# Kernel optimization log

Measured on AMD Instinct MI355X. Metric: run time of the kernel, lower is better.

The kernel has to match this reference:

```python
import jax, jax.numpy as jnp
import numpy as np

B, N, C = 2, 2048, 768
H = 12
D = C // H
SCALE = D ** -0.5
EPS = 1e-5
HID = 4 * C


def layer_norm(x, g, b):
    mu = jnp.mean(x, axis=-1, keepdims=True)
    var = jnp.var(x, axis=-1, keepdims=True)
    return (x - mu) * jax.lax.rsqrt(var + EPS) * g + b


def setup_inputs():
    key = jax.random.key(0)
    ks = jax.random.split(key, 12)
    s = C ** -0.5
    x = jax.random.normal(ks[0], (B, N, C), dtype=jnp.float32)
    mask = (jax.random.uniform(ks[1], (B, N, N)) < 0.1).astype(jnp.float32)
    return {
        "x": x,
        "mask": mask,
        "g1": jnp.ones((C,), jnp.float32),
        "b1": jnp.zeros((C,), jnp.float32),
        "Wq": jax.random.normal(ks[2], (C, C), jnp.float32) * s,
        "Wkv": jax.random.normal(ks[3], (2 * C, C), jnp.float32) * s,
        "Wp": jax.random.normal(ks[4], (C, C), jnp.float32) * s,
        "bp": jnp.zeros((C,), jnp.float32),
        "g2": jnp.ones((C,), jnp.float32),
        "b2": jnp.zeros((C,), jnp.float32),
        "W1": jax.random.normal(ks[5], (HID, C), jnp.float32) * s,
        "bf1": jnp.zeros((HID,), jnp.float32),
        "W2": jax.random.normal(ks[6], (C, HID), jnp.float32) * (HID ** -0.5),
        "bf2": jnpmp if False else jnp.zeros((C,), jnp.float32),
    }


def block_fwd(x, mask, g1, b1, Wq, Wkv, Wp, bp, g2, b2, W1, bf1, W2, bf2):
    # --- attention branch (pre-norm) ---
    xn = layer_norm(x, g1, b1)
    q = (xn @ Wq.T).reshape(B, N, H, D).transpose(0, 2, 1, 3)      # bhnd
    kv = (xn @ Wkv.T).reshape(B, N, 2, H, D).transpose(2, 0, 3, 1, 4)
    k, v = kv[0], kv[1]                                             # bhnd
    attn = jnp.einsum('bhnd,bhmd->bhnm', q, k) * SCALE
    attn = attn + (mask * -100000.0)[:, None]                       # additive mask
    attn = jax.nn.softmax(attn, axis=-1)
    o = jnp.einsum('bhnm,bhmd->bhnd', attn, v)
    o = o.transpose(0, 2, 1, 3).reshape(B, N, C)
    o = o @ Wp.T + bp
    x = x + o
    # --- MLP branch (pre-norm) ---
    xn2 = layer_norm(x, g2, b2)
    h = jax.nn.gelu(xn2 @ W1.T + bf1, approximate=False)
    x = x + (h @ W2.T + bf2)
    return x


def reference(x, mask, g1, b1, Wq, Wkv, Wp, bp, g2, b2, W1, bf1, W2, bf2):
    return block_fwd(x, mask, g1, b1, Wq, Wkv, Wp, bp, g2, b2, W1, bf1, W2, bf2)
```

## Files before the change

kernel.cpp:

```cpp
#include <hip/hip_runtime.h>
#include <hip/hip_bf16.h>
#include <cstdint>
#include <cstddef>

#define BB 2
#define NN 2048
#define CC 768
#define HH 12
#define DD 64
#define HID 3072
#define TT (BB*NN)

typedef __attribute__((ext_vector_type(8))) short bf16x8;
typedef __attribute__((ext_vector_type(4))) short bf16x4;
typedef __attribute__((ext_vector_type(4))) float f32x4;

__device__ __forceinline__ unsigned short f2bf(float f) {
    unsigned int u = __float_as_uint(f);
    u += 0x7fffu + ((u >> 16) & 1u);
    return (unsigned short)(u >> 16);
}
__device__ __forceinline__ float bf2f(unsigned short u) {
    return __uint_as_float(((unsigned int)u) << 16);
}
#if __has_builtin(__builtin_amdgcn_exp2f)
#define EXP2F(x) __builtin_amdgcn_exp2f(x)
#else
#define EXP2F(x) exp2f(x)
#endif

__device__ __forceinline__ void gload16(const void* g, void* l) {
    __builtin_amdgcn_global_load_lds((__attribute__((address_space(1))) unsigned int*)g,
                                     (__attribute__((address_space(3))) unsigned int*)l,
                                     16, 0, 0);
}

__device__ __forceinline__ void barrier_lgkm() {
    asm volatile("s_waitcnt lgkmcnt(0)" ::: "memory");
    __builtin_amdgcn_s_barrier();
}

struct CvtArgs {
    const float* in[5];
    unsigned short* out[5];
    int n4[5];
};
typedef __attribute__((ext_vector_type(4))) float float4v;
typedef __attribute__((ext_vector_type(4))) unsigned short ushort4v;
__global__ __launch_bounds__(256) void cvt5_kernel(CvtArgs a) {
    int base = blockIdx.x * 256 + threadIdx.x;
    int stride = gridDim.x * 256;
#pragma unroll
    for (int s = 0; s < 5; ++s) {
        const float4v* ip = (const float4v*)a.in[s];
        ushort4v* op = (ushort4v*)a.out[s];
        for (int i = base; i < a.n4[s]; i += stride) {
            float4v v = ip[i];
            ushort4v o;
            o[0] = f2bf(v[0]); o[1] = f2bf(v[1]); o[2] = f2bf(v[2]); o[3] = f2bf(v[3]);
            op[i] = o;
        }
    }
}

__global__ __launch_bounds__(256) void maskbits_kernel(const float* __restrict__ mask,
                                                       unsigned short* __restrict__ mb, int n) {
    int i = blockIdx.x * 256 + threadIdx.x;
    if (i >= n) return;
    const float4v* mp = (const float4v*)(mask + (size_t)i * 16);
    unsigned int bits = 0;
#pragma unroll
    for (int q = 0; q < 4; ++q) {
        float4v v = mp[q];
#pragma unroll
        for (int j = 0; j < 4; ++j) bits |= (v[j] > 0.5f) ? (1u << (q * 4 + j)) : 0u;
    }
    mb[i] = (unsigned short)bits;
}

__global__ __launch_bounds__(256) void ln_kernel(const float* __restrict__ x,
                                                 const float* __restrict__ g,
                                                 const float* __restrict__ b,
                                                 unsigned short* __restrict__ out) {
    int t = blockIdx.x;
    int tid = threadIdx.x;
    const float* xr = x + (size_t)t * CC;
    float v0 = xr[tid], v1 = xr[tid + 256], v2 = xr[tid + 512];
    float s = v0 + v1 + v2;
    float s2 = v0 * v0 + v1 * v1 + v2 * v2;
#pragma unroll
    for (int off = 1; off < 64; off <<= 1) {
        s  += __shfl_xor(s, off);
        s2 += __shfl_xor(s2, off);
    }
    __shared__ float red[8];
    int wv = tid >> 6, lane = tid & 63;
    if (lane == 0) { red[wv] = s; red[wv + 4] = s2; }
    __syncthreads();
    s  = red[0] + red[1] + red[2] + red[3];
    s2 = red[4] + red[5] + red[6] + red[7];
    float mu   = s * (1.0f / CC);
    float var  = s2 * (1.0f / CC) - mu * mu;
    float rstd = rsqrtf(var + 1e-5f);
    unsigned short* orow = out + (size_t)t * CC;
    orow[tid]       = f2bf((v0 - mu) * rstd * g[tid]       + b[tid]);
    orow[tid + 256] = f2bf((v1 - mu) * rstd * g[tid + 256] + b[tid + 256]);
    orow[tid + 512] = f2bf((v2 - mu) * rstd * g[tid + 512] + b[tid + 512]);
}

template <int EPI, int BM>
__global__ __launch_bounds__(256) void gemm_bt(const unsigned short* __restrict__ A,
                                               const unsigned short* __restrict__ Bw,
                                               const float* __restrict__ bias,
                                               const float* __restrict__ res,
                                               void* __restrict__ out,
                                               int M, int N, int K) {
    constexpr int MI = BM / 32;
    __shared__ alignas(16) unsigned short As[BM * 32];
    __shared__ alignas(16) unsigned short Bs[128 * 32];
    int tid = threadIdx.x;
    int lane = tid & 63, wv = tid >> 6;
    int l16 = lane & 15, lg = lane >> 4;
    int bm = blockIdx.x, bn = blockIdx.y;
    int wm = (wv & 1) * (BM / 2), wn = (wv >> 1) * 64;

    f32x4 acc[MI][4];
#pragma unroll
    for (int i = 0; i < MI; ++i)
#pragma unroll
        for (int j = 0; j < 4; ++j) acc[i][j] = f32x4{0.f, 0.f, 0.f, 0.f};

    const unsigned short* Ab = A + (size_t)bm * BM * K;
    const unsigned short* Bb = Bw + (size_t)bn * 128 * K;

    for (int k0 = 0; k0 < K; k0 += 32) {
        __syncthreads();
        constexpr int NCA = (BM * 4) / 256;
#pragma unroll
        for (int i = 0; i < NCA; ++i) {
            int c = tid + i * 256;
            int row = c >> 2, cc = (c & 3) * 8;
            gload16(Ab + (size_t)row * K + k0 + cc, &As[c * 8]);
        }
#pragma unroll
        for (int i = 0; i < 2; ++i) {
            int c = tid + i * 256;
            int row = c >> 2, cc = (c & 3) * 8;
            gload16(Bb + (size_t)row * K + k0 + cc, &Bs[c * 8]);
        }
        __syncthreads();
        bf16x8 af[MI], bfr[4];
#pragma unroll
        for (int mi = 0; mi < MI; ++mi) af[mi]  = *(const bf16x8*)&As[(wm + mi * 16 + l16) * 32 + lg * 8];
#pragma unroll
        for (int ni = 0; ni < 4; ++ni) bfr[ni] = *(const bf16x8*)&Bs[(wn + ni * 16 + l16) * 32 + lg * 8];
#pragma unroll
        for (int mi = 0; mi < MI; ++mi)
#pragma unroll
            for (int ni = 0; ni < 4; ++ni)
                acc[mi][ni] = __builtin_amdgcn_mfma_f32_16x16x32_bf16(af[mi], bfr[ni], acc[mi][ni], 0, 0, 0);
    }

#pragma unroll
    for (int ni = 0; ni < 4; ++ni) {
        int col = bn * 128 + wn + ni * 16 + l16;
        float bv = (EPI == 0) ? 0.f : bias[col];
#pragma unroll
        for (int mi = 0; mi < MI; ++mi) {
#pragma unroll
            for (int r = 0; r < 4; ++r) {
                int row = bm * BM + wm + mi * 16 + lg * 4 + r;
                float v = acc[mi][ni][r];
                size_t idx = (size_t)row * N + col;
                if (EPI == 0) {
                    ((unsigned short*)out)[idx] = f2bf(v);
                } else if (EPI == 1) {
                    ((float*)out)[idx] = v + bv + res[idx];
                } else if (EPI == 2) {
                    v += bv;
                    v = 0.5f * v * (1.0f + erff(v * 0.70710678118f));
                    ((unsigned short*)out)[idx] = f2bf(v);
                } else {
                    ((float*)out)[idx] = v + bv + res[idx];
                }
            }
        }
    }
}

#define KVB 64
#define ANT (NN/KVB)
#define VP 68
__global__ __launch_bounds__(256) void attn_kernel(const unsigned short* __restrict__ qkv,
                                                   const unsigned short* __restrict__ maskb,
                                                   unsigned short* __restrict__ o) {
    __shared__ alignas(16) unsigned short Ks[2][64 * 64];
    __shared__ alignas(16) unsigned short Vt[2][64 * VP];
    int tid = threadIdx.x;
    int lane = tid & 63, wv = tid >> 6;
    int l16 = lane & 15, lg = lane >> 4;
    int qb = blockIdx.x;
    int bh = blockIdx.y;
    int b = bh / HH, h = bh % HH;
    int qrow = qb * 64 + wv * 16 + l16;

    const unsigned short* qp = qkv + ((size_t)(b * NN + qrow)) * 2304 + h * DD;
    bf16x8 q0r = *(const bf16x8*)(qp + 8 * lg);
    bf16x8 q1r = *(const bf16x8*)(qp + 32 + 8 * lg);
    const float QSC = 0.125f * 1.4426950408889634f;
    bf16x8 q0, q1;
#pragma unroll
    for (int j = 0; j < 8; ++j) {
        q0[j] = (short)f2bf(bf2f((unsigned short)q0r[j]) * QSC);
        q1[j] = (short)f2bf(bf2f((unsigned short)q1r[j]) * QSC);
    }

    const unsigned short* mrow  = maskb + ((size_t)(b * NN + qrow)) * 128;
    const unsigned short* kbase = qkv + (size_t)b * NN * 2304 + 768 + h * DD;
    const unsigned short* vbase = qkv + (size_t)b * NN * 2304 + 1536 + h * DD;

    int kc1_row = tid >> 3, kc7 = tid & 7;
    int kc2_row = kc1_row + 32;
    int klds1 = kc1_row * 64 + ((kc7 ^ (kc1_row & 7)) * 8);
    int klds2 = kc2_row * 64 + ((kc7 ^ (kc2_row & 7)) * 8);
    int kp = tid & 31, dg = tid >> 5;

    int sw = l16 & 7;
    int kb0 = l16 * 64 + ((lg ^ sw) * 8);
    int kb1 = l16 * 64 + (((lg + 4) ^ sw) * 8);
    int vbo = l16 * VP + lg * 4;

    bf16x8 ka, kb, va, vb;
    unsigned long long mb_cur, mb_nxt;

    f32x4 oa[4];
#pragma unroll
    for (int i = 0; i < 4; ++i) oa[i] = f32x4{0.f, 0.f, 0.f, 0.f};
    float mrun = -INFINITY, lrun = 0.f;

    auto LOAD = [&](int t) {
        ka = *(const bf16x8*)(kbase + (size_t)(t * KVB + kc1_row) * 2304 + kc7 * 8);
        kb = *(const bf16x8*)(kbase + (size_t)(t * KVB + kc2_row) * 2304 + kc7 * 8);
        va = *(const bf16x8*)(vbase + (size_t)(t * KVB + 2 * kp) * 2304 + dg * 8);
        vb = *(const bf16x8*)(vbase + (size_t)(t * KVB + 2 * kp + 1) * 2304 + dg * 8);
        mb_nxt = *(const unsigned long long*)(mrow + t * 4);
    };
    auto WRITE = [&](int s) {
        unsigned short* Kd = Ks[s];
        *(bf16x8*)&Kd[klds1] = ka;
        *(bf16x8*)&Kd[klds2] = kb;
        unsigned int* VtU = (unsigned int*)Vt[s];
#pragma unroll
        for (int j = 0; j < 8; ++j)
            VtU[(dg * 8 + j) * (VP / 2) + kp] =
                (unsigned int)(unsigned short)va[j] | ((unsigned int)(unsigned short)vb[j] << 16);
    };

    LOAD(0);
    WRITE(0);
    mb_cur = mb_nxt;
    int cur = 0;

    for (int kt = 0; kt < ANT; ++kt) {
        bool pre = (kt + 1 < ANT);
        if (pre) LOAD(kt + 1);
        barrier_lgkm();
        const unsigned short* Ksc = Ks[cur];
        const unsigned short* Vtc = Vt[cur];

        float sv[16];
#pragma unroll
        for (int ks = 0; ks < 4; ++ks) {
            bf16x8 k0 = *(const bf16x8*)&Ksc[kb0 + ks * 1024];
            bf16x8 k1 = *(const bf16x8*)&Ksc[kb1 + ks * 1024];
            f32x4 sa = f32x4{0.f, 0.f, 0.f, 0.f};
            sa = __builtin_amdgcn_mfma_f32_16x16x32_bf16(k0, q0, sa, 0, 0, 0);
            sa = __builtin_amdgcn_mfma_f32_16x16x32_bf16(k1, q1, sa, 0, 0, 0);
            unsigned int m16 = (unsigned int)(mb_cur >> (ks * 16 + lg * 4));
#pragma unroll
            for (int r = 0; r < 4; ++r) {
                float mbit = (float)((m16 >> r) & 1u);
                sv[ks * 4 + r] = fmaf(mbit, -144269.5f, sa[r]);
            }
        }
        float tmax = sv[0];
#pragma unroll
        for (int i = 1; i < 16; ++i) tmax = fmaxf(tmax, sv[i]);
        tmax = fmaxf(tmax, __shfl_xor(tmax, 16));
        tmax = fmaxf(tmax, __shfl_xor(tmax, 32));

        if (__any(tmax > mrun + 11.5f)) {
            float mnew = fmaxf(mrun, tmax);
            float sc = EXP2F(mrun - mnew);
            lrun *= sc;
#pragma unroll
            for (int db = 0; db < 4; ++db) {
                oa[db][0] *= sc; oa[db][1] *= sc; oa[db][2] *= sc; oa[db][3] *= sc;
            }
            mrun = mnew;
        }

        float ps = 0.f;
        bf16x4 pf[4];
#pragma unroll
        for (int ks = 0; ks < 4; ++ks)
#pragma unroll
            for (int r = 0; r < 4; ++r) {
                float p = EXP2F(sv[ks * 4 + r] - mrun);
                ps += p;
                pf[ks][r] = (short)f2bf(p);
            }
        lrun += ps;

#pragma unroll
        for (int ks = 0; ks < 4; ++ks)
#pragma unroll
            for (int db = 0; db < 4; ++db) {
                bf16x4 vf = *(const bf16x4*)&Vtc[vbo + db * 16 * VP + ks * 16];
                oa[db] = __builtin_amdgcn_mfma_f32_16x16x16bf16_1k(vf, pf[ks], oa[db], 0, 0, 0);
            }

        barrier_lgkm();
        if (pre) { WRITE(cur ^ 1); cur ^= 1; mb_cur = mb_nxt; }
    }

    float lt = lrun;
    lt += __shfl_xor(lt, 16);
    lt += __shfl_xor(lt, 32);
    float inv = 1.0f / lt;
    unsigned short* op = o + ((size_t)(b * NN + qrow)) * CC + h * DD;
#pragma unroll
    for (int db = 0; db < 4; ++db) {
        bf16x4 ov;
#pragma unroll
        for (int r = 0; r < 4; ++r) ov[r] = (short)f2bf(oa[db][r] * inv);
        *(bf16x4*)&op[db * 16 + lg * 4] = ov;
    }
}

extern "C" void kernel_launch(void* const* d_in, const int* in_sizes, int n_in,
                              void* d_out, int out_size, void* d_ws, size_t ws_size,
                              hipStream_t stream) {
    const float* x    = (const float*)d_in[0];
    const float* mask = (const float*)d_in[1];
    const float* g1   = (const float*)d_in[2];
    const float* b1   = (const float*)d_in[3];
    const float* Wq   = (const float*)d_in[4];
    const float* Wkv  = (const float*)d_in[5];
    const float* Wp   = (const float*)d_in[6];
    const float* bp   = (const float*)d_in[7];
    const float* g2   = (const float*)d_in[8];
    const float* b2   = (const float*)d_in[9];
    const float* W1   = (const float*)d_in[10];
    const float* bf1  = (const float*)d_in[11];
    const float* W2   = (const float*)d_in[12];
    const float* bf2  = (const float*)d_in[13];
    float* out = (float*)d_out;

    char* w = (char*)d_ws;
    unsigned short* wqkv = (unsigned short*)w;      w += (size_t)2304 * 768 * 2;
    unsigned short* wp   = (unsigned short*)w;      w += (size_t)768 * 768 * 2;
    unsigned short* w1   = (unsigned short*)w;      w += (size_t)3072 * 768 * 2;
    unsigned short* w2   = (unsigned short*)w;      w += (size_t)768 * 3072 * 2;
    unsigned short* xn   = (unsigned short*)w;      w += (size_t)TT * CC * 2;
    unsigned short* qkv  = (unsigned short*)w;      w += (size_t)TT * 2304 * 2;
    unsigned short* mb   = (unsigned short*)w;      w += (size_t)BB * NN * 128 * 2;
    unsigned short* obuf = (unsigned short*)w;      w += (size_t)TT * CC * 2;
    float*          x1   = (float*)w;               w += (size_t)TT * CC * 4;
    unsigned short* xn2  = (unsigned short*)w;      w += (size_t)TT * CC * 2;
    unsigned short* hbuf = (unsigned short*)w;      w += (size_t)TT * HID * 2;

    CvtArgs ca;
    ca.in[0] = Wq;  ca.out[0] = wqkv;             ca.n4[0] = 768 * 768 / 4;
    ca.in[1] = Wkv; ca.out[1] = wqkv + 768 * 768; ca.n4[1] = 1536 * 768 / 4;
    ca.in[2] = Wp;  ca.out[2] = wp;               ca.n4[2] = 768 * 768 / 4;
    ca.in[3] = W1;  ca.out[3] = w1;               ca.n4[3] = 3072 * 768 / 4;
    ca.in[4] = W2;  ca.out[4] = w2;               ca.n4[4] = 768 * 3072 / 4;
    cvt5_kernel<<<1024, 256, 0, stream>>>(ca);

    {
        int n = BB * NN * (NN / 16);
        maskbits_kernel<<<(n + 255) / 256, 256, 0, stream>>>(mask, mb, n);
    }

    ln_kernel<<<TT, 256, 0, stream>>>(x, g1, b1, xn);

    gemm_bt<0, 128><<<dim3(TT / 128, 2304 / 128), 256, 0, stream>>>(xn, wqkv, nullptr, nullptr, qkv, TT, 2304, 768);

    attn_kernel<<<dim3(NN / 64, BB * HH), 256, 0, stream>>>(qkv, mb, obuf);

    gemm_bt<1, 64><<<dim3(TT / 64, 768 / 128), 256, 0, stream>>>(obuf, wp, bp, x, x1, TT, 768, 768);

    ln_kernel<<<TT, 256, 0, stream>>>(x1, g2, b2, xn2);

    gemm_bt<2, 128><<<dim3(TT / 128, HID / 128), 256, 0, stream>>>(xn2, w1, bf1, nullptr, hbuf, TT, HID, 768);

    gemm_bt<3, 64><<<dim3(TT / 64, 768 / 128), 256, 0, stream>>>(hbuf, w2, bf2, x1, out, TT, 768, HID);
}
```

Before: 226.8 us.

## Double-buffer GEMM LDS with swizzle and widen attention to 512 threads

The GEMM now double-buffers its A/B LDS tiles, issuing the next k-slice's direct-to-LDS loads before computing the current one, and XOR-swizzles the column chunks to cut LDS bank conflicts. It needs one barrier per iteration instead of two. The attention kernel moves to 512-thread blocks covering 128 query rows, which halves K/V tile loads per query. K tiles now go straight to LDS via global_load_lds, while V is still transposed through registers. This costs more LDS per GEMM block and larger attention blocks, which can lower occupancy, and it depends on the global_load_lds completing before the __syncthreads.

```diff
diff --git a/kernel.cpp b/kernel.cpp
--- a/kernel.cpp
+++ b/kernel.cpp
@@ -33,11 +33,6 @@
     __builtin_amdgcn_global_load_lds((__attribute__((address_space(1))) unsigned int*)g,
                                      (__attribute__((address_space(3))) unsigned int*)l,
                                      16, 0, 0);
-}
-
-__device__ __forceinline__ void barrier_lgkm() {
-    asm volatile("s_waitcnt lgkmcnt(0)" ::: "memory");
-    __builtin_amdgcn_s_barrier();
 }
 
 struct CvtArgs {
@@ -116,49 +111,69 @@
                                                void* __restrict__ out,
                                                int M, int N, int K) {
     constexpr int MI = BM / 32;
-    __shared__ alignas(16) unsigned short As[BM * 32];
-    __shared__ alignas(16) unsigned short Bs[128 * 32];
+    constexpr int NCA = (BM * 4) / 256;
+    __shared__ alignas(16) unsigned short As[2][BM * 32];
+    __shared__ alignas(16) unsigned short Bs[2][128 * 32];
     int tid = threadIdx.x;
     int lane = tid & 63, wv = tid >> 6;
     int l16 = lane & 15, lg = lane >> 4;
     int bm = blockIdx.x, bn = blockIdx.y;
     int wm = (wv & 1) * (BM / 2), wn = (wv >> 1) * 64;
 
-    f32x4 acc[MI][4];
-#pragma unroll
-    for (int i = 0; i < MI; ++i)
-#pragma unroll
-        for (int j = 0; j < 4; ++j) acc[i][j] = f32x4{0.f, 0.f, 0.f, 0.f};
-
     const unsigned short* Ab = A + (size_t)bm * BM * K;
     const unsigned short* Bb = Bw + (size_t)bn * 128 * K;
 
-    for (int k0 = 0; k0 < K; k0 += 32) {
-        __syncthreads();
-        constexpr int NCA = (BM * 4) / 256;
-#pragma unroll
-        for (int i = 0; i < NCA; ++i) {
-            int c = tid + i * 256;
-            int row = c >> 2, cc = (c & 3) * 8;
-            gload16(Ab + (size_t)row * K + k0 + cc, &As[c * 8]);
-        }
-#pragma unroll
-        for (int i = 0; i < 2; ++i) {
-            int c = tid + i * 256;
-            int row = c >> 2, cc = (c & 3) * 8;
-            gload16(Bb + (size_t)row * K + k0 + cc, &Bs[c * 8]);
-        }
-        __syncthreads();
+    const unsigned short* aSrc[NCA]; int aDst[NCA];
+#pragma unroll
+    for (int i = 0; i < NCA; ++i) {
+        int c = tid + i * 256;
+        int row = c >> 2, p = c & 3;
+        int lc = p ^ ((row >> 1) & 3);
+        aSrc[i] = Ab + (size_t)row * K + lc * 8;
+        aDst[i] = c * 8;
+    }
+    const unsigned short* bSrc[2]; int bDst[2];
+#pragma unroll
+    for (int i = 0; i < 2; ++i) {
+        int c = tid + i * 256;
+        int row = c >> 2, p = c & 3;
+        int lc = p ^ ((row >> 1) & 3);
+        bSrc[i] = Bb + (size_t)row * K + lc * 8;
+        bDst[i] = c * 8;
+    }
+    int aoff = (wm + l16) * 32 + ((lg ^ (((wm + l16) >> 1) & 3)) * 8);
+    int boff = (wn + l16) * 32 + ((lg ^ (((wn + l16) >> 1) & 3)) * 8);
+
+    f32x4 acc[MI][4];
+#pragma unroll
+    for (int i = 0; i < MI; ++i)
+#pragma unroll
+        for (int j = 0; j < 4; ++j) acc[i][j] = f32x4{0.f, 0.f, 0.f, 0.f};
+
+    auto STAGE = [&](int s, int k0) {
+#pragma unroll
+        for (int i = 0; i < NCA; ++i) gload16(aSrc[i] + k0, &As[s][aDst[i]]);
+#pragma unroll
+        for (int i = 0; i < 2; ++i)   gload16(bSrc[i] + k0, &Bs[s][bDst[i]]);
+    };
+
+    STAGE(0, 0);
+    __syncthreads();
+    int nt = K / 32;
+    for (int t = 0; t < nt; ++t) {
+        int cur = t & 1;
+        if (t + 1 < nt) STAGE(cur ^ 1, (t + 1) * 32);
         bf16x8 af[MI], bfr[4];
 #pragma unroll
-        for (int mi = 0; mi < MI; ++mi) af[mi]  = *(const bf16x8*)&As[(wm + mi * 16 + l16) * 32 + lg * 8];
-#pragma unroll
-        for (int ni = 0; ni < 4; ++ni) bfr[ni] = *(const bf16x8*)&Bs[(wn + ni * 16 + l16) * 32 + lg * 8];
+        for (int mi = 0; mi < MI; ++mi) af[mi]  = *(const bf16x8*)&As[cur][aoff + mi * 512];
+#pragma unroll
+        for (int ni = 0; ni < 4; ++ni)  bfr[ni] = *(const bf16x8*)&Bs[cur][boff + ni * 512];
 #pragma unroll
         for (int mi = 0; mi < MI; ++mi)
 #pragma unroll
             for (int ni = 0; ni < 4; ++ni)
                 acc[mi][ni] = __builtin_amdgcn_mfma_f32_16x16x32_bf16(af[mi], bfr[ni], acc[mi][ni], 0, 0, 0);
+        __syncthreads();
     }
 
 #pragma unroll
@@ -191,7 +206,7 @@
 #define KVB 64
 #define ANT (NN/KVB)
 #define VP 68
-__global__ __launch_bounds__(256) void attn_kernel(const unsigned short* __restrict__ qkv,
+__global__ __launch_bounds__(512) void attn_kernel(const unsigned short* __restrict__ qkv,
                                                    const unsigned short* __restrict__ maskb,
                                                    unsigned short* __restrict__ o) {
     __shared__ alignas(16) unsigned short Ks[2][64 * 64];
@@ -202,7 +217,7 @@
     int qb = blockIdx.x;
     int bh = blockIdx.y;
     int b = bh / HH, h = bh % HH;
-    int qrow = qb * 64 + wv * 16 + l16;
+    int qrow = qb * 128 + wv * 16 + l16;
 
     const unsigned short* qp = qkv + ((size_t)(b * NN + qrow)) * 2304 + h * DD;
     bf16x8 q0r = *(const bf16x8*)(qp + 8 * lg);
@@ -219,18 +234,18 @@
     const unsigned short* kbase = qkv + (size_t)b * NN * 2304 + 768 + h * DD;
     const unsigned short* vbase = qkv + (size_t)b * NN * 2304 + 1536 + h * DD;
 
-    int kc1_row = tid >> 3, kc7 = tid & 7;
-    int kc2_row = kc1_row + 32;
-    int klds1 = kc1_row * 64 + ((kc7 ^ (kc1_row & 7)) * 8);
-    int klds2 = kc2_row * 64 + ((kc7 ^ (kc2_row & 7)) * 8);
+    int k_row = tid >> 3, k_p = tid & 7;
+    int k_lc = k_p ^ (k_row & 7);
+    const unsigned short* kSrc = kbase + (size_t)k_row * 2304 + k_lc * 8;
     int kp = tid & 31, dg = tid >> 5;
+    const unsigned short* vSrc = vbase + (size_t)(2 * kp) * 2304 + dg * 4;
 
     int sw = l16 & 7;
     int kb0 = l16 * 64 + ((lg ^ sw) * 8);
     int kb1 = l16 * 64 + (((lg + 4) ^ sw) * 8);
     int vbo = l16 * VP + lg * 4;
 
-    bf16x8 ka, kb, va, vb;
+    bf16x4 va, vb;
     unsigned long long mb_cur, mb_nxt;
 
     f32x4 oa[4];
@@ -238,33 +253,30 @@
     for (int i = 0; i < 4; ++i) oa[i] = f32x4{0.f, 0.f, 0.f, 0.f};
     float mrun = -INFINITY, lrun = 0.f;
 
-    auto LOAD = [&](int t) {
-        ka = *(const bf16x8*)(kbase + (size_t)(t * KVB + kc1_row) * 2304 + kc7 * 8);
-        kb = *(const bf16x8*)(kbase + (size_t)(t * KVB + kc2_row) * 2304 + kc7 * 8);
-        va = *(const bf16x8*)(vbase + (size_t)(t * KVB + 2 * kp) * 2304 + dg * 8);
-        vb = *(const bf16x8*)(vbase + (size_t)(t * KVB + 2 * kp + 1) * 2304 + dg * 8);
+    auto LOAD = [&](int t, int s) {
+        gload16(kSrc + (size_t)t * KVB * 2304, &Ks[s][tid * 8]);
+        const unsigned short* vp = vSrc + (size_t)t * KVB * 2304;
+        va = *(const bf16x4*)(vp);
+        vb = *(const bf16x4*)(vp + 2304);
         mb_nxt = *(const unsigned long long*)(mrow + t * 4);
     };
-    auto WRITE = [&](int s) {
-        unsigned short* Kd = Ks[s];
-        *(bf16x8*)&Kd[klds1] = ka;
-        *(bf16x8*)&Kd[klds2] = kb;
+    auto WRITEV = [&](int s) {
         unsigned int* VtU = (unsigned int*)Vt[s];
 #pragma unroll
-        for (int j = 0; j < 8; ++j)
-            VtU[(dg * 8 + j) * (VP / 2) + kp] =
+        for (int j = 0; j < 4; ++j)
+            VtU[(dg * 4 + j) * (VP / 2) + kp] =
                 (unsigned int)(unsigned short)va[j] | ((unsigned int)(unsigned short)vb[j] << 16);
     };
 
-    LOAD(0);
-    WRITE(0);
+    LOAD(0, 0);
+    WRITEV(0);
     mb_cur = mb_nxt;
+    __syncthreads();
     int cur = 0;
 
     for (int kt = 0; kt < ANT; ++kt) {
         bool pre = (kt + 1 < ANT);
-        if (pre) LOAD(kt + 1);
-        barrier_lgkm();
+        if (pre) LOAD(kt + 1, cur ^ 1);
         const unsigned short* Ksc = Ks[cur];
         const unsigned short* Vtc = Vt[cur];
 
@@ -320,8 +332,9 @@
                 oa[db] = __builtin_amdgcn_mfma_f32_16x16x16bf16_1k(vf, pf[ks], oa[db], 0, 0, 0);
             }
 
-        barrier_lgkm();
-        if (pre) { WRITE(cur ^ 1); cur ^= 1; mb_cur = mb_nxt; }
+        if (pre) WRITEV(cur ^ 1);
+        __syncthreads();
+        if (pre) { cur ^= 1; mb_cur = mb_nxt; }
     }
 
     float lt = lrun;
@@ -387,7 +400,7 @@
 
     gemm_bt<0, 128><<<dim3(TT / 128, 2304 / 128), 256, 0, stream>>>(xn, wqkv, nullptr, nullptr, qkv, TT, 2304, 768);
 
-    attn_kernel<<<dim3(NN / 64, BB * HH), 256, 0, stream>>>(qkv, mb, obuf);
+    attn_kernel<<<dim3(NN / 128, BB * HH), 512, 0, stream>>>(qkv, mb, obuf);
 
     gemm_bt<1, 64><<<dim3(TT / 64, 768 / 128), 256, 0, stream>>>(obuf, wp, bp, x, x1, TT, 768, 768);
 
```

Result: no change. 228.1 us (+0.6%).
